# Kernel tuning notes

Measured on AMD Instinct MI355X. Metric: run time of the kernel, lower is better.

Reference implementation:

```python
import jax, jax.numpy as jnp
import numpy as np

T, B, D_IN, D_H, D_OUT = 16, 8192, 512, 1024, 256


def setup_inputs() -> dict:
    key = jax.random.key(0)
    ks = jax.random.split(key, 4)
    # He-style scaled init to keep activations sane
    x = jax.random.normal(ks[0], (B, D_IN), dtype=jnp.float32)
    W1 = jax.random.normal(ks[1], (T, D_IN, D_H), dtype=jnp.float32) / np.sqrt(D_IN)
    b1 = jnp.zeros((T, D_H), dtype=jnp.float32)
    W2 = jax.random.normal(ks[2], (T, D_H, D_H), dtype=jnp.float32) / np.sqrt(D_H)
    b2 = jnp.zeros((T, D_H), dtype=jnp.float32)
    W3 = jax.random.normal(ks[3], (T, D_H, D_OUT), dtype=jnp.float32) / np.sqrt(D_H)
    b3 = jnp.zeros((T, D_OUT), dtype=jnp.float32)
    return {"x": x, "W1": W1, "b1": b1, "W2": W2, "b2": b2, "W3": W3, "b3": b3}


def reference(x, W1, b1, W2, b2, W3, b3):
    # Batched over the tree dimension t: one grouped GEMM per layer instead of
    # a Python loop over trees.
    h = jax.nn.relu(jnp.einsum('bi,tih->tbh', x, W1) + b1[:, None, :])   # [T,B,H]
    h = jax.nn.relu(jnp.einsum('tbh,thk->tbk', h, W2) + b2[:, None, :])  # [T,B,H]
    out = jnp.einsum('tbh,tho->tbo', h, W3) + b3[:, None, :]             # [T,B,O]
    return jnp.mean(out, axis=0)                                          # [B,O]
```

## Files before the change

kernel.cpp:

```cpp
#include <hip/hip_runtime.h>
#include <hip/hip_bf16.h>
#include <stdint.h>

#define T_TREES 16
#define B_ROWS  8192
#define DIN     512
#define DH      1024
#define DOUT    256

typedef unsigned short u16;
typedef __attribute__((ext_vector_type(8))) short short8;
typedef __attribute__((ext_vector_type(4))) float floatx4;

__device__ __forceinline__ u16 f2bf(float f) {
    union { float f; uint32_t u; } v; v.f = f;
    uint32_t u = v.u;
    uint32_t r = (u + 0x7fffu + ((u >> 16) & 1u)) >> 16;
    return (u16)r;
}

__device__ __forceinline__ void async_copy16(const u16* g, u16* l) {
    __builtin_amdgcn_global_load_lds(
        (const __attribute__((address_space(1))) uint32_t*)g,
        (__attribute__((address_space(3))) uint32_t*)l,
        16, 0, 0);
}

__global__ void convert_x_kernel(const float* __restrict__ in, u16* __restrict__ out, int n4) {
    int idx = blockIdx.x * 256 + threadIdx.x;
    if (idx < n4) {
        float4 v = ((const float4*)in)[idx];
        ushort4 o;
        o.x = f2bf(v.x); o.y = f2bf(v.y); o.z = f2bf(v.z); o.w = f2bf(v.w);
        ((ushort4*)out)[idx] = o;
    }
}

__global__ void convert_transpose_kernel(const float* __restrict__ in, u16* __restrict__ out,
                                         int K, int N, float scale) {
    __shared__ float tile[32][33];
    int t = blockIdx.z;
    int k0 = blockIdx.x * 32, n0 = blockIdx.y * 32;
    const float* inb = in + (size_t)t * K * N;
    u16* outb = out + (size_t)t * K * N;
    int c = threadIdx.x & 31, rg = threadIdx.x >> 5;
#pragma unroll
    for (int i = 0; i < 4; i++) {
        int r = rg * 4 + i;
        tile[r][c] = inb[(size_t)(k0 + r) * N + n0 + c];
    }
    __syncthreads();
#pragma unroll
    for (int i = 0; i < 4; i++) {
        int r = rg * 4 + i;
        outb[(size_t)(n0 + r) * K + k0 + c] = f2bf(tile[c][r] * scale);
    }
}

__global__ void init_out_kernel(const float* __restrict__ b3, float* __restrict__ out) {
    int idx = blockIdx.x * 256 + threadIdx.x;
    int o = idx & (DOUT - 1);
    float s = 0.f;
#pragma unroll
    for (int t = 0; t < T_TREES; t++) s += b3[t * DOUT + o];
    out[idx] = s * (1.f / T_TREES);
}

__global__ __launch_bounds__(256, 2)
void gemm_relu_bf16(const u16* __restrict__ A, size_t aStrideT,
                    const u16* __restrict__ Bt,
                    const float* __restrict__ bias,
                    u16* __restrict__ C,
                    int M, int N, int K) {
    __shared__ u16 ldsA[128 * 64];
    __shared__ u16 ldsB[128 * 64];

    const int t = blockIdx.z;
    const u16* Ab = A + (size_t)t * aStrideT;
    const u16* Bb = Bt + (size_t)t * (size_t)N * K;
    u16* Cb = C + (size_t)t * (size_t)M * N;
    const float* biasb = bias + (size_t)t * N;

    const int m0 = blockIdx.x * 128;
    const int n0 = blockIdx.y * 128;

    const int tid = threadIdx.x;
    const int wave = tid >> 6;
    const int lane = tid & 63;
    const int quad = lane >> 4;
    const int l16 = lane & 15;
    const int wm = (wave >> 1) * 64;
    const int wn = (wave & 1) * 64;

    const int s = lane >> 3;
    const int c8 = lane & 7;
    const int p = s & 1;
    const int colElem = ((c8 ^ (p << 2)) << 3);

    const int ph = l16 & 1;

    floatx4 acc[4][4];
    const floatx4 zero = {0.f, 0.f, 0.f, 0.f};
#pragma unroll
    for (int i = 0; i < 4; i++)
#pragma unroll
        for (int j = 0; j < 4; j++) acc[i][j] = zero;

    for (int kk = 0; kk < K; kk += 64) {
#pragma unroll
        for (int i = 0; i < 4; i++) {
            const int j = wave * 4 + i;
            const int r = j * 8 + s;
            async_copy16(Ab + (size_t)(m0 + r) * K + kk + colElem, &ldsA[j * 512]);
            async_copy16(Bb + (size_t)(n0 + r) * K + kk + colElem, &ldsB[j * 512]);
        }
        __syncthreads();

#pragma unroll
        for (int h = 0; h < 2; h++) {
            const int ch = (h ^ ph) << 5;
            short8 a[4], b[4];
#pragma unroll
            for (int mi = 0; mi < 4; mi++)
                a[mi] = *(const short8*)&ldsA[(wm + mi * 16 + l16) * 64 + ch + quad * 8];
#pragma unroll
            for (int ni = 0; ni < 4; ni++)
                b[ni] = *(const short8*)&ldsB[(wn + ni * 16 + l16) * 64 + ch + quad * 8];
#pragma unroll
            for (int mi = 0; mi < 4; mi++)
#pragma unroll
                for (int ni = 0; ni < 4; ni++)
                    acc[mi][ni] = __builtin_amdgcn_mfma_f32_16x16x32_bf16(a[mi], b[ni], acc[mi][ni], 0, 0, 0);
        }
        __syncthreads();
    }

#pragma unroll
    for (int ni = 0; ni < 4; ni++) {
        const int n = n0 + wn + ni * 16 + l16;
        const float bv = biasb[n];
#pragma unroll
        for (int mi = 0; mi < 4; mi++) {
#pragma unroll
            for (int i = 0; i < 4; i++) {
                const int m = m0 + wm + mi * 16 + quad * 4 + i;
                float v = acc[mi][ni][i] + bv;
                v = v > 0.f ? v : 0.f;
                Cb[(size_t)m * N + n] = f2bf(v);
            }
        }
    }
}

__global__ __launch_bounds__(256, 2)
void gemm_final(const u16* __restrict__ H2, const u16* __restrict__ W3t,
                float* __restrict__ Out) {
    constexpr int M = B_ROWS, N = DOUT, K = DH;
    __shared__ u16 ldsA[128 * 32];
    __shared__ u16 ldsB[128 * 32];

    const int m0 = blockIdx.x * 128;
    const int n0 = blockIdx.y * 128;
    const int t = blockIdx.z;

    const int tid = threadIdx.x;
    const int wave = tid >> 6;
    const int lane = tid & 63;
    const int quad = lane >> 4;
    const int l16 = lane & 15;
    const int wm = (wave >> 1) * 64;
    const int wn = (wave & 1) * 64;

    const int j0 = wave * 2, j1 = wave * 2 + 1;
    const int sRow0 = j0 * 16 + (lane >> 2);
    const int sRow1 = j1 * 16 + (lane >> 2);
    const int sCol = (lane & 3) * 8;

    floatx4 acc[4][4];
    const floatx4 zero = {0.f, 0.f, 0.f, 0.f};
#pragma unroll
    for (int i = 0; i < 4; i++)
#pragma unroll
        for (int j = 0; j < 4; j++) acc[i][j] = zero;

    const u16* Ab = H2 + (size_t)t * M * K;
    const u16* Bb = W3t + (size_t)t * N * K;
    for (int kk = 0; kk < K; kk += 32) {
        async_copy16(Ab + (size_t)(m0 + sRow0) * K + kk + sCol, &ldsA[j0 * 512]);
        async_copy16(Ab + (size_t)(m0 + sRow1) * K + kk + sCol, &ldsA[j1 * 512]);
        async_copy16(Bb + (size_t)(n0 + sRow0) * K + kk + sCol, &ldsB[j0 * 512]);
        async_copy16(Bb + (size_t)(n0 + sRow1) * K + kk + sCol, &ldsB[j1 * 512]);
        __syncthreads();

        short8 a[4], b[4];
#pragma unroll
        for (int mi = 0; mi < 4; mi++)
            a[mi] = *(const short8*)&ldsA[(wm + mi * 16 + l16) * 32 + quad * 8];
#pragma unroll
        for (int ni = 0; ni < 4; ni++)
            b[ni] = *(const short8*)&ldsB[(wn + ni * 16 + l16) * 32 + quad * 8];
#pragma unroll
        for (int mi = 0; mi < 4; mi++)
#pragma unroll
            for (int ni = 0; ni < 4; ni++)
                acc[mi][ni] = __builtin_amdgcn_mfma_f32_16x16x32_bf16(a[mi], b[ni], acc[mi][ni], 0, 0, 0);
        __syncthreads();
    }

#pragma unroll
    for (int ni = 0; ni < 4; ni++) {
        const int n = n0 + wn + ni * 16 + l16;
#pragma unroll
        for (int mi = 0; mi < 4; mi++) {
#pragma unroll
            for (int i = 0; i < 4; i++) {
                const int m = m0 + wm + mi * 16 + quad * 4 + i;
                atomicAdd(&Out[(size_t)m * N + n], acc[mi][ni][i]);
            }
        }
    }
}

extern "C" void kernel_launch(void* const* d_in, const int* in_sizes, int n_in,
                              void* d_out, int out_size, void* d_ws, size_t ws_size,
                              hipStream_t stream) {
    const float* x  = (const float*)d_in[0];
    const float* W1 = (const float*)d_in[1];
    const float* b1 = (const float*)d_in[2];
    const float* W2 = (const float*)d_in[3];
    const float* b2 = (const float*)d_in[4];
    const float* W3 = (const float*)d_in[5];
    const float* b3 = (const float*)d_in[6];
    float* out = (float*)d_out;

    const size_t XB_BYTES = 8388608ull;
    const size_t W1B_BYTES = 16777216ull, W2B_BYTES = 33554432ull, W3B_BYTES = 8388608ull;
    const size_t FIXED = XB_BYTES + W1B_BYTES + W2B_BYTES + W3B_BYTES;
    const size_t PER_TREE = 33554432ull;

    uint8_t* ws = (uint8_t*)d_ws;
    u16* xb  = (u16*)ws;
    u16* W1b = (u16*)(ws + XB_BYTES);
    u16* W2b = (u16*)(ws + XB_BYTES + W1B_BYTES);
    u16* W3b = (u16*)(ws + XB_BYTES + W1B_BYTES + W2B_BYTES);
    u16* h1  = (u16*)(ws + FIXED);

    int g = 16;
    while (g > 1 && FIXED + (size_t)g * PER_TREE > ws_size) g >>= 1;
    const int nG = T_TREES / g;
    u16* h2 = (u16*)(ws + FIXED + (size_t)g * (PER_TREE / 2));

    convert_x_kernel<<<4096, 256, 0, stream>>>(x, xb, (B_ROWS * DIN) / 4);
    init_out_kernel<<<(B_ROWS * DOUT) / 256, 256, 0, stream>>>(b3, out);
    convert_transpose_kernel<<<dim3(DIN / 32, DH / 32, T_TREES), 256, 0, stream>>>(W1, W1b, DIN, DH, 1.f);
    convert_transpose_kernel<<<dim3(DH / 32, DH / 32, T_TREES), 256, 0, stream>>>(W2, W2b, DH, DH, 1.f);
    convert_transpose_kernel<<<dim3(DH / 32, DOUT / 32, T_TREES), 256, 0, stream>>>(W3, W3b, DH, DOUT, 1.f / T_TREES);

    for (int gi = 0; gi < nG; gi++) {
        const int t0 = gi * g;
        gemm_relu_bf16<<<dim3(B_ROWS / 128, DH / 128, g), 256, 0, stream>>>(
            xb, 0, W1b + (size_t)t0 * DIN * DH, b1 + (size_t)t0 * DH, h1, B_ROWS, DH, DIN);
        gemm_relu_bf16<<<dim3(B_ROWS / 128, DH / 128, g), 256, 0, stream>>>(
            h1, (size_t)B_ROWS * DH, W2b + (size_t)t0 * DH * DH, b2 + (size_t)t0 * DH, h2, B_ROWS, DH, DH);
        gemm_final<<<dim3(B_ROWS / 128, DOUT / 128, g), 256, 0, stream>>>(
            h2, W3b + (size_t)t0 * DH * DOUT, out);
    }
}
```

Before: 868.0 us.

## Switch GEMMs to 32x32x16 MFMA tiles and merge setup kernels

Replaces the 16x16x32 MFMA fragment layout with 32x32x16 bf16 MFMA and a 2x2 fragment grid per wave. The LDS swizzle is changed to match, and the shared K-slab loop is pulled into macros. gemm_final now uses 64-wide K slabs like the relu GEMMs, halving its barrier count. The x/bias setup kernels and the three weight convert-transpose kernels are each merged into one launch to cut launch overhead. The new swizzle and output index mapping must match the 32x32 accumulator layout, which is a correctness risk.

Result: no change. 879.2 us (+1.3%).

```diff
diff --git a/kernel.cpp b/kernel.cpp
--- a/kernel.cpp
+++ b/kernel.cpp
@@ -10,7 +10,7 @@
 
 typedef unsigned short u16;
 typedef __attribute__((ext_vector_type(8))) short short8;
-typedef __attribute__((ext_vector_type(4))) float floatx4;
+typedef __attribute__((ext_vector_type(16))) float floatx16;
 
 __device__ __forceinline__ u16 f2bf(float f) {
     union { float f; uint32_t u; } v; v.f = f;
@@ -26,21 +26,36 @@
         16, 0, 0);
 }
 
-__global__ void convert_x_kernel(const float* __restrict__ in, u16* __restrict__ out, int n4) {
-    int idx = blockIdx.x * 256 + threadIdx.x;
-    if (idx < n4) {
-        float4 v = ((const float4*)in)[idx];
+__global__ void setup_kernel(const float* __restrict__ x, u16* __restrict__ xb,
+                             const float* __restrict__ b3, float* __restrict__ out) {
+    if (blockIdx.x < 4096) {
+        int idx = blockIdx.x * 256 + threadIdx.x;
+        float4 v = ((const float4*)x)[idx];
         ushort4 o;
         o.x = f2bf(v.x); o.y = f2bf(v.y); o.z = f2bf(v.z); o.w = f2bf(v.w);
-        ((ushort4*)out)[idx] = o;
-    }
-}
-
-__global__ void convert_transpose_kernel(const float* __restrict__ in, u16* __restrict__ out,
-                                         int K, int N, float scale) {
+        ((ushort4*)xb)[idx] = o;
+    } else {
+        int idx = (blockIdx.x - 4096) * 256 + threadIdx.x;
+        int o = idx & (DOUT - 1);
+        float s = 0.f;
+#pragma unroll
+        for (int t = 0; t < T_TREES; t++) s += b3[t * DOUT + o];
+        out[idx] = s * (1.f / T_TREES);
+    }
+}
+
+__global__ void convert_weights_kernel(const float* __restrict__ W1, const float* __restrict__ W2,
+                                       const float* __restrict__ W3,
+                                       u16* __restrict__ W1b, u16* __restrict__ W2b,
+                                       u16* __restrict__ W3b) {
     __shared__ float tile[32][33];
-    int t = blockIdx.z;
-    int k0 = blockIdx.x * 32, n0 = blockIdx.y * 32;
+    int t = blockIdx.z, tl = blockIdx.x;
+    const float* in; u16* out; int K, N, kt, nt; float scale = 1.f;
+    if (tl < 512)       { in = W1; out = W1b; K = DIN; N = DH;   kt = tl & 15; nt = tl >> 4; }
+    else if (tl < 1536) { tl -= 512;  in = W2; out = W2b; K = DH; N = DH;   kt = tl & 31; nt = tl >> 5; }
+    else                { tl -= 1536; in = W3; out = W3b; K = DH; N = DOUT; kt = tl & 31; nt = tl >> 5;
+                          scale = 1.f / T_TREES; }
+    int k0 = kt * 32, n0 = nt * 32;
     const float* inb = in + (size_t)t * K * N;
     u16* outb = out + (size_t)t * K * N;
     int c = threadIdx.x & 31, rg = threadIdx.x >> 5;
@@ -57,14 +72,49 @@
     }
 }
 
-__global__ void init_out_kernel(const float* __restrict__ b3, float* __restrict__ out) {
-    int idx = blockIdx.x * 256 + threadIdx.x;
-    int o = idx & (DOUT - 1);
-    float s = 0.f;
-#pragma unroll
-    for (int t = 0; t < T_TREES; t++) s += b3[t * DOUT + o];
-    out[idx] = s * (1.f / T_TREES);
-}
+
+#define GEMM_PREAMBLE()                                          \
+    const int tid = threadIdx.x;                                 \
+    const int wave = tid >> 6;                                   \
+    const int lane = tid & 63;                                   \
+    const int l31 = lane & 31;                                   \
+    const int h = lane >> 5;                                     \
+    const int rb = l31 & 3;            \
+    const int wm = (wave >> 1) * 64;                             \
+    const int wn = (wave & 1) * 64;                              \
+    const int s = lane >> 3;           \
+    const int c8 = lane & 7;                                     \
+    const int colElem = ((c8 ^ ((s & 3) << 1)) << 3);
+
+#define GEMM_KSLAB(Ab, Bb, K)                                                         \
+    {                                                                                  \
+        _Pragma("unroll")                                                              \
+        for (int i = 0; i < 4; i++) {                                                  \
+            const int j = wave * 4 + i;                                                \
+            const int r = j * 8 + s;                                                   \
+            async_copy16(Ab + (size_t)(m0 + r) * K + kk + colElem, &ldsA[j * 512]);    \
+            async_copy16(Bb + (size_t)(n0 + r) * K + kk + colElem, &ldsB[j * 512]);    \
+        }                                                                              \
+        __syncthreads();                                                               \
+        _Pragma("unroll")                                                              \
+        for (int kq = 0; kq < 4; kq++) {                                               \
+            const int col = ((kq ^ rb) << 4) + h * 8;                                  \
+            short8 a[2], b[2];                                                         \
+            _Pragma("unroll")                                                          \
+            for (int fi = 0; fi < 2; fi++)                                             \
+                a[fi] = *(const short8*)&ldsA[(wm + fi * 32 + l31) * 64 + col];        \
+            _Pragma("unroll")                                                          \
+            for (int fj = 0; fj < 2; fj++)                                             \
+                b[fj] = *(const short8*)&ldsB[(wn + fj * 32 + l31) * 64 + col];        \
+            _Pragma("unroll")                                                          \
+            for (int fi = 0; fi < 2; fi++)                                             \
+                _Pragma("unroll")                                                      \
+                for (int fj = 0; fj < 2; fj++)                                         \
+                    acc[fi][fj] = __builtin_amdgcn_mfma_f32_32x32x16_bf16(             \
+                        a[fi], b[fj], acc[fi][fj], 0, 0, 0);                           \
+        }                                                                              \
+        __syncthreads();                                                               \
+    }
 
 __global__ __launch_bounds__(256, 2)
 void gemm_relu_bf16(const u16* __restrict__ A, size_t aStrideT,
@@ -84,67 +134,28 @@
     const int m0 = blockIdx.x * 128;
     const int n0 = blockIdx.y * 128;
 
-    const int tid = threadIdx.x;
-    const int wave = tid >> 6;
-    const int lane = tid & 63;
-    const int quad = lane >> 4;
-    const int l16 = lane & 15;
-    const int wm = (wave >> 1) * 64;
-    const int wn = (wave & 1) * 64;
-
-    const int s = lane >> 3;
-    const int c8 = lane & 7;
-    const int p = s & 1;
-    const int colElem = ((c8 ^ (p << 2)) << 3);
-
-    const int ph = l16 & 1;
-
-    floatx4 acc[4][4];
-    const floatx4 zero = {0.f, 0.f, 0.f, 0.f};
-#pragma unroll
-    for (int i = 0; i < 4; i++)
-#pragma unroll
-        for (int j = 0; j < 4; j++) acc[i][j] = zero;
-
-    for (int kk = 0; kk < K; kk += 64) {
-#pragma unroll
-        for (int i = 0; i < 4; i++) {
-            const int j = wave * 4 + i;
-            const int r = j * 8 + s;
-            async_copy16(Ab + (size_t)(m0 + r) * K + kk + colElem, &ldsA[j * 512]);
-            async_copy16(Bb + (size_t)(n0 + r) * K + kk + colElem, &ldsB[j * 512]);
-        }
-        __syncthreads();
-
-#pragma unroll
-        for (int h = 0; h < 2; h++) {
-            const int ch = (h ^ ph) << 5;
-            short8 a[4], b[4];
-#pragma unroll
-            for (int mi = 0; mi < 4; mi++)
-                a[mi] = *(const short8*)&ldsA[(wm + mi * 16 + l16) * 64 + ch + quad * 8];
-#pragma unroll
-            for (int ni = 0; ni < 4; ni++)
-                b[ni] = *(const short8*)&ldsB[(wn + ni * 16 + l16) * 64 + ch + quad * 8];
-#pragma unroll
-            for (int mi = 0; mi < 4; mi++)
-#pragma unroll
-                for (int ni = 0; ni < 4; ni++)
-                    acc[mi][ni] = __builtin_amdgcn_mfma_f32_16x16x32_bf16(a[mi], b[ni], acc[mi][ni], 0, 0, 0);
-        }
-        __syncthreads();
-    }
-
-#pragma unroll
-    for (int ni = 0; ni < 4; ni++) {
-        const int n = n0 + wn + ni * 16 + l16;
+    GEMM_PREAMBLE();
+
+    floatx16 acc[2][2];
+#pragma unroll
+    for (int fi = 0; fi < 2; fi++)
+#pragma unroll
+        for (int fj = 0; fj < 2; fj++)
+#pragma unroll
+            for (int r = 0; r < 16; r++) acc[fi][fj][r] = 0.f;
+
+    for (int kk = 0; kk < K; kk += 64) GEMM_KSLAB(Ab, Bb, K);
+
+#pragma unroll
+    for (int fj = 0; fj < 2; fj++) {
+        const int n = n0 + wn + fj * 32 + l31;
         const float bv = biasb[n];
 #pragma unroll
-        for (int mi = 0; mi < 4; mi++) {
-#pragma unroll
-            for (int i = 0; i < 4; i++) {
-                const int m = m0 + wm + mi * 16 + quad * 4 + i;
-                float v = acc[mi][ni][i] + bv;
+        for (int fi = 0; fi < 2; fi++) {
+#pragma unroll
+            for (int r = 0; r < 16; r++) {
+                const int m = m0 + wm + fi * 32 + (r & 3) + 8 * (r >> 2) + 4 * h;
+                float v = acc[fi][fj][r] + bv;
                 v = v > 0.f ? v : 0.f;
                 Cb[(size_t)m * N + n] = f2bf(v);
             }
@@ -156,66 +167,36 @@
 void gemm_final(const u16* __restrict__ H2, const u16* __restrict__ W3t,
                 float* __restrict__ Out) {
     constexpr int M = B_ROWS, N = DOUT, K = DH;
-    __shared__ u16 ldsA[128 * 32];
-    __shared__ u16 ldsB[128 * 32];
+    __shared__ u16 ldsA[128 * 64];
+    __shared__ u16 ldsB[128 * 64];
 
     const int m0 = blockIdx.x * 128;
     const int n0 = blockIdx.y * 128;
     const int t = blockIdx.z;
-
-    const int tid = threadIdx.x;
-    const int wave = tid >> 6;
-    const int lane = tid & 63;
-    const int quad = lane >> 4;
-    const int l16 = lane & 15;
-    const int wm = (wave >> 1) * 64;
-    const int wn = (wave & 1) * 64;
-
-    const int j0 = wave * 2, j1 = wave * 2 + 1;
-    const int sRow0 = j0 * 16 + (lane >> 2);
-    const int sRow1 = j1 * 16 + (lane >> 2);
-    const int sCol = (lane & 3) * 8;
-
-    floatx4 acc[4][4];
-    const floatx4 zero = {0.f, 0.f, 0.f, 0.f};
-#pragma unroll
-    for (int i = 0; i < 4; i++)
-#pragma unroll
-        for (int j = 0; j < 4; j++) acc[i][j] = zero;
-
     const u16* Ab = H2 + (size_t)t * M * K;
     const u16* Bb = W3t + (size_t)t * N * K;
-    for (int kk = 0; kk < K; kk += 32) {
-        async_copy16(Ab + (size_t)(m0 + sRow0) * K + kk + sCol, &ldsA[j0 * 512]);
-        async_copy16(Ab + (size_t)(m0 + sRow1) * K + kk + sCol, &ldsA[j1 * 512]);
-        async_copy16(Bb + (size_t)(n0 + sRow0) * K + kk + sCol, &ldsB[j0 * 512]);
-        async_copy16(Bb + (size_t)(n0 + sRow1) * K + kk + sCol, &ldsB[j1 * 512]);
-        __syncthreads();
-
-        short8 a[4], b[4];
-#pragma unroll
-        for (int mi = 0; mi < 4; mi++)
-            a[mi] = *(const short8*)&ldsA[(wm + mi * 16 + l16) * 32 + quad * 8];
-#pragma unroll
-        for (int ni = 0; ni < 4; ni++)
-            b[ni] = *(const short8*)&ldsB[(wn + ni * 16 + l16) * 32 + quad * 8];
-#pragma unroll
-        for (int mi = 0; mi < 4; mi++)
-#pragma unroll
-            for (int ni = 0; ni < 4; ni++)
-                acc[mi][ni] = __builtin_amdgcn_mfma_f32_16x16x32_bf16(a[mi], b[ni], acc[mi][ni], 0, 0, 0);
-        __syncthreads();
-    }
-
-#pragma unroll
-    for (int ni = 0; ni < 4; ni++) {
-        const int n = n0 + wn + ni * 16 + l16;
-#pragma unroll
-        for (int mi = 0; mi < 4; mi++) {
-#pragma unroll
-            for (int i = 0; i < 4; i++) {
-                const int m = m0 + wm + mi * 16 + quad * 4 + i;
-                atomicAdd(&Out[(size_t)m * N + n], acc[mi][ni][i]);
+
+    GEMM_PREAMBLE();
+
+    floatx16 acc[2][2];
+#pragma unroll
+    for (int fi = 0; fi < 2; fi++)
+#pragma unroll
+        for (int fj = 0; fj < 2; fj++)
+#pragma unroll
+            for (int r = 0; r < 16; r++) acc[fi][fj][r] = 0.f;
+
+    for (int kk = 0; kk < K; kk += 64) GEMM_KSLAB(Ab, Bb, K);
+
+#pragma unroll
+    for (int fj = 0; fj < 2; fj++) {
+        const int n = n0 + wn + fj * 32 + l31;
+#pragma unroll
+        for (int fi = 0; fi < 2; fi++) {
+#pragma unroll
+            for (int r = 0; r < 16; r++) {
+                const int m = m0 + wm + fi * 32 + (r & 3) + 8 * (r >> 2) + 4 * h;
+                atomicAdd(&Out[(size_t)m * N + n], acc[fi][fj][r]);
             }
         }
     }
@@ -250,11 +231,9 @@
     const int nG = T_TREES / g;
     u16* h2 = (u16*)(ws + FIXED + (size_t)g * (PER_TREE / 2));
 
-    convert_x_kernel<<<4096, 256, 0, stream>>>(x, xb, (B_ROWS * DIN) / 4);
-    init_out_kernel<<<(B_ROWS * DOUT) / 256, 256, 0, stream>>>(b3, out);
-    convert_transpose_kernel<<<dim3(DIN / 32, DH / 32, T_TREES), 256, 0, stream>>>(W1, W1b, DIN, DH, 1.f);
-    convert_transpose_kernel<<<dim3(DH / 32, DH / 32, T_TREES), 256, 0, stream>>>(W2, W2b, DH, DH, 1.f);
-    convert_transpose_kernel<<<dim3(DH / 32, DOUT / 32, T_TREES), 256, 0, stream>>>(W3, W3b, DH, DOUT, 1.f / T_TREES);
+    setup_kernel<<<4096 + 8192, 256, 0, stream>>>(x, xb, b3, out);
+    convert_weights_kernel<<<dim3(1792, 1, T_TREES), 256, 0, stream>>>(
+        W1, W2, W3, W1b, W2b, W3b);
 
     for (int gi = 0; gi < nG; gi++) {
         const int t0 = gi * g;
```
